# Performance work log

Measured on AMD Instinct MI355X. Metric: run time of the kernel, lower is better.

The kernel has to match this reference:

```python
import jax, jax.numpy as jnp
import numpy as np

D_MODEL = 1024


def setup_inputs() -> dict:
    key = jax.random.key(0)
    k1, k2, k3, k4, k5, k6 = jax.random.split(key, 6)
    B, S, D = 4, 4096, D_MODEL
    scale = 1.0 / np.sqrt(D)
    return {
        "hidden": jax.random.normal(k1, (B, S, D), dtype=jnp.float32),
        "pre_emb": jax.random.normal(k2, (B, S, D), dtype=jnp.float32),
        "w1": jax.random.normal(k3, (D, D), dtype=jnp.float32) * scale,  # [in, out]
        "b1": jax.random.normal(k4, (D,), dtype=jnp.float32) * 0.01,
        "w2": jax.random.normal(k5, (D, D), dtype=jnp.float32) * scale,
        "b2": jax.random.normal(k6, (D,), dtype=jnp.float32) * 0.01,
    }


def reference(hidden, pre_emb, w1, b1, w2, b2):
    # h = Linear1(hidden); i = Linear2(hidden + pre_emb)
    h = jnp.einsum("bsd,de->bse", hidden, w1) + b1            # [B,S,D]
    i = jnp.einsum("bsd,de->bse", hidden + pre_emb, w2) + b2  # [B,S,D]
    attn = jnp.einsum("bqd,bkd->bqk", h, i)                   # [B,S,S]
    return jax.nn.softmax(attn, axis=-1)
```

## Files before the change

### kernel.cpp

```cpp
#include <hip/hip_runtime.h>
#include <hip/hip_bf16.h>
#include <stdint.h>

#define DM   1024
#define BATCH 4
#define SEQ  4096
#define MTOT (BATCH*SEQ)

typedef __attribute__((ext_vector_type(8))) short bf16x8;
typedef __attribute__((ext_vector_type(4))) float f32x4;

#define GLOAD_LDS16(gp, lp) __builtin_amdgcn_global_load_lds( \
    (const __attribute__((address_space(1))) unsigned int*)(gp), \
    (__attribute__((address_space(3))) unsigned int*)(lp), 16, 0, 0)

__device__ __forceinline__ ushort f2bf(float f){
  uint u = __float_as_uint(f);
  u += 0x7FFFu + ((u >> 16) & 1u);
  return (ushort)(u >> 16);
}
__device__ __forceinline__ float bf2f(ushort b){ return __uint_as_float(((uint)b) << 16); }

__device__ __forceinline__ void split4(const float4 v, ushort4& h4, ushort4& l4){
  h4.x = f2bf(v.x); l4.x = f2bf(v.x - bf2f(h4.x));
  h4.y = f2bf(v.y); l4.y = f2bf(v.y - bf2f(h4.y));
  h4.z = f2bf(v.z); l4.z = f2bf(v.z - bf2f(h4.z));
  h4.w = f2bf(v.w); l4.w = f2bf(v.w - bf2f(h4.w));
}

__global__ __launch_bounds__(256)
void prep_w_split(const float* __restrict__ w1, const float* __restrict__ w2,
                  ushort* __restrict__ w1h, ushort* __restrict__ w1l,
                  ushort* __restrict__ w2h, ushort* __restrict__ w2l){
  const float* w = blockIdx.y ? w2 : w1;
  ushort* oh = blockIdx.y ? w2h : w1h;
  ushort* ol = blockIdx.y ? w2l : w1l;
  size_t off = ((size_t)blockIdx.x * 256 + threadIdx.x) * 4;
  float4 v = *(const float4*)&w[off];
  ushort4 h4, l4; split4(v, h4, l4);
  *(ushort4*)&oh[off] = h4;
  *(ushort4*)&ol[off] = l4;
}

__global__ __launch_bounds__(256)
void prep_xy(const float* __restrict__ hidden, const float* __restrict__ pre,
             ushort* __restrict__ xh, ushort* __restrict__ xl,
             ushort* __restrict__ yh, ushort* __restrict__ yl, int writeX){
  size_t off = ((size_t)blockIdx.x * 256 + threadIdx.x) * 4;
  float4 h = *(const float4*)&hidden[off];
  float4 p = *(const float4*)&pre[off];
  float4 y = {h.x + p.x, h.y + p.y, h.z + p.z, h.w + p.w};
  ushort4 a, b;
  if (writeX){
    split4(h, a, b);
    *(ushort4*)&xh[off] = a;
    *(ushort4*)&xl[off] = b;
  }
  split4(y, a, b);
  *(ushort4*)&yh[off] = a;
  *(ushort4*)&yl[off] = b;
}

__global__ __launch_bounds__(256)
void c2k(const float* __restrict__ w2, const float* __restrict__ b1,
         float* __restrict__ c2){
  const int wid = threadIdx.x >> 6, lane = threadIdx.x & 63;
  const int row = blockIdx.x * 4 + wid;
  float s = 0.f;
  #pragma unroll
  for (int t = 0; t < 16; t++){
    int e = lane + 64 * t;
    s += w2[(size_t)row * DM + e] * b1[e];
  }
  #pragma unroll
  for (int o = 32; o > 0; o >>= 1) s += __shfl_xor(s, o, 64);
  if (lane == 0) c2[row] = s;
}

__global__ __launch_bounds__(256)
void betak(const ushort* __restrict__ yh, const ushort* __restrict__ yl,
           const float* __restrict__ c2, float* __restrict__ beta){
  const int wid = threadIdx.x >> 6, lane = threadIdx.x & 63;
  const size_t r = (size_t)blockIdx.x * 4 + wid;
  const size_t base = r * DM + lane * 16;
  float s = 0.f;
  #pragma unroll
  for (int q = 0; q < 2; q++){
    bf16x8 h = *(const bf16x8*)&yh[base + q * 8];
    bf16x8 l = *(const bf16x8*)&yl[base + q * 8];
    float4 c0 = *(const float4*)&c2[lane * 16 + q * 8];
    float4 c1 = *(const float4*)&c2[lane * 16 + q * 8 + 4];
    s += (bf2f((ushort)h[0]) + bf2f((ushort)l[0])) * c0.x;
    s += (bf2f((ushort)h[1]) + bf2f((ushort)l[1])) * c0.y;
    s += (bf2f((ushort)h[2]) + bf2f((ushort)l[2])) * c0.z;
    s += (bf2f((ushort)h[3]) + bf2f((ushort)l[3])) * c0.w;
    s += (bf2f((ushort)h[4]) + bf2f((ushort)l[4])) * c1.x;
    s += (bf2f((ushort)h[5]) + bf2f((ushort)l[5])) * c1.y;
    s += (bf2f((ushort)h[6]) + bf2f((ushort)l[6])) * c1.z;
    s += (bf2f((ushort)h[7]) + bf2f((ushort)l[7])) * c1.w;
  }
  #pragma unroll
  for (int o = 32; o > 0; o >>= 1) s += __shfl_xor(s, o, 64);
  if (lane == 0) beta[r] = s;
}

__device__ __forceinline__ void bt_mainloop(
    const ushort* __restrict__ Aph, const ushort* __restrict__ Apl,
    const ushort* __restrict__ Bph, const ushort* __restrict__ Bpl,
    int m0, int n0, f32x4 (&acc)[4][4]){
  __shared__ alignas(16) ushort Ah[128*32];
  __shared__ alignas(16) ushort Al[128*32];
  __shared__ alignas(16) ushort Bh[128*32];
  __shared__ alignas(16) ushort Bl[128*32];

  const int tid = threadIdx.x;
  const int lane = tid & 63, wid = tid >> 6;
  const int wm = (wid & 1) * 64, wn = (wid >> 1) * 64;
  const int lr = lane & 15, lk = (lane >> 4) * 8;

  const ushort* plane = (wid == 0) ? Aph : (wid == 1) ? Apl : (wid == 2) ? Bph : Bpl;
  ushort* lds = (wid == 0) ? Ah : (wid == 1) ? Al : (wid == 2) ? Bh : Bl;
  const int r0 = (wid < 2) ? m0 : n0;
  const size_t goff = (size_t)(r0 + (lane >> 2)) * DM + (lane & 3) * 8;

  for (int k0 = 0; k0 < DM; k0 += 32){
    __syncthreads();
    const ushort* gp = plane + goff + k0;
    #pragma unroll
    for (int t = 0; t < 8; t++){
      GLOAD_LDS16(gp + (size_t)t * 16 * DM, lds + t * 512);
    }
    __syncthreads();

    bf16x8 fah[4], fal[4], fbh[4], fbl[4];
    #pragma unroll
    for (int i = 0; i < 4; i++){
      fah[i] = *(const bf16x8*)&Ah[(wm + i*16 + lr)*32 + lk];
      fal[i] = *(const bf16x8*)&Al[(wm + i*16 + lr)*32 + lk];
      fbh[i] = *(const bf16x8*)&Bh[(wn + i*16 + lr)*32 + lk];
      fbl[i] = *(const bf16x8*)&Bl[(wn + i*16 + lr)*32 + lk];
    }
    #pragma unroll
    for (int i = 0; i < 4; i++)
      #pragma unroll
      for (int j = 0; j < 4; j++){
        acc[i][j] = __builtin_amdgcn_mfma_f32_16x16x32_bf16(fah[i], fbh[j], acc[i][j], 0, 0, 0);
        acc[i][j] = __builtin_amdgcn_mfma_f32_16x16x32_bf16(fah[i], fbl[j], acc[i][j], 0, 0, 0);
        acc[i][j] = __builtin_amdgcn_mfma_f32_16x16x32_bf16(fal[i], fbh[j], acc[i][j], 0, 0, 0);
      }
  }
}

__global__ __launch_bounds__(256, 2)
void gemm_bt_split(const ushort* __restrict__ Aph, const ushort* __restrict__ Apl,
                   const ushort* __restrict__ Bph, const ushort* __restrict__ Bpl,
                   ushort* __restrict__ oh, ushort* __restrict__ ol){
  const int m0 = blockIdx.y * 128, n0 = blockIdx.x * 128;
  f32x4 acc[4][4];
  for (int i = 0; i < 4; i++) for (int j = 0; j < 4; j++) acc[i][j] = (f32x4){0.f,0.f,0.f,0.f};
  bt_mainloop(Aph, Apl, Bph, Bpl, m0, n0, acc);

  const int lane = threadIdx.x & 63, wid = threadIdx.x >> 6;
  const int wm = (wid & 1) * 64, wn = (wid >> 1) * 64;
  const int lr = lane & 15;
  const int rbase = (lane >> 4) * 4;
  #pragma unroll
  for (int i = 0; i < 4; i++)
    #pragma unroll
    for (int j = 0; j < 4; j++){
      int gc = n0 + wn + j*16 + lr;
      #pragma unroll
      for (int r = 0; r < 4; r++){
        int gr = m0 + wm + i*16 + rbase + r;
        float v = acc[i][j][r];
        ushort hb = f2bf(v);
        size_t o = (size_t)gr * DM + gc;
        oh[o] = hb;
        ol[o] = f2bf(v - bf2f(hb));
      }
    }
}

__global__ __launch_bounds__(256, 2)
void gemm_bt_f32(const ushort* __restrict__ Aph, const ushort* __restrict__ Apl,
                 const ushort* __restrict__ Bph, const ushort* __restrict__ Bpl,
                 float* __restrict__ out){
  const int b = blockIdx.y;
  const int id = blockIdx.x;
  const int c = id & 7;
  const int m = (id >> 3) & 63;
  const int s = m >> 3, u = m & 7;
  const int g = id >> 9;
  const int qt = 16*g + 8*(c & 1) + s;
  const int kt = 8*(c >> 1) + u;
  const int m0 = qt * 128, n0 = kt * 128;
  const size_t abase = (size_t)b * SEQ * DM;

  f32x4 acc[4][4];
  for (int i = 0; i < 4; i++) for (int j = 0; j < 4; j++) acc[i][j] = (f32x4){0.f,0.f,0.f,0.f};
  bt_mainloop(Aph + abase, Apl + abase, Bph + abase, Bpl + abase, m0, n0, acc);

  const int lane = threadIdx.x & 63, wid = threadIdx.x >> 6;
  const int wm = (wid & 1) * 64, wn = (wid >> 1) * 64;
  const int lr = lane & 15;
  const int rbase = (lane >> 4) * 4;
  #pragma unroll
  for (int i = 0; i < 4; i++)
    #pragma unroll
    for (int j = 0; j < 4; j++){
      int gc = n0 + wn + j*16 + lr;
      #pragma unroll
      for (int r = 0; r < 4; r++){
        int gr = m0 + wm + i*16 + rbase + r;
        __builtin_nontemporal_store(acc[i][j][r],
            &out[((size_t)b * SEQ + gr) * SEQ + gc]);
      }
    }
}

#define ASTR 40
__global__ __launch_bounds__(256, 2)
void gemm_z_manual(const float* __restrict__ hidden,
                   const ushort* __restrict__ gth, const ushort* __restrict__ gtl,
                   ushort* __restrict__ zh, ushort* __restrict__ zl){
  const int m0 = blockIdx.y * 128, n0 = blockIdx.x * 128;
  __shared__ alignas(16) ushort Ah[128*ASTR];
  __shared__ alignas(16) ushort Al[128*ASTR];
  __shared__ alignas(16) ushort Bh[128*32];
  __shared__ alignas(16) ushort Bl[128*32];

  const int tid = threadIdx.x;
  const int lane = tid & 63, wid = tid >> 6;
  const int wm = (wid & 1) * 64, wn = (wid >> 1) * 64;
  const int lr = lane & 15, lk = (lane >> 4) * 8;

  const ushort* bp = (wid < 2) ? gth : gtl;
  ushort* blds = (wid < 2) ? Bh : Bl;
  const int tb = (wid & 1) * 4;
  const size_t bgoff = (size_t)(n0 + (lane >> 2)) * DM + (lane & 3) * 8;

  f32x4 acc[4][4];
  for (int i = 0; i < 4; i++) for (int j = 0; j < 4; j++) acc[i][j] = (f32x4){0.f,0.f,0.f,0.f};

  for (int k0 = 0; k0 < DM; k0 += 32){
    __syncthreads();
    const ushort* gb = bp + bgoff + k0;
    #pragma unroll
    for (int t = 0; t < 4; t++){
      GLOAD_LDS16(gb + (size_t)(tb + t) * 16 * DM, blds + (tb + t) * 512);
    }
    #pragma unroll
    for (int c = 0; c < 4; c++){
      int idx = c * 256 + tid;
      int row = idx >> 3, kq = (idx & 7) * 4;
      size_t ga = (size_t)(m0 + row) * DM + k0 + kq;
      float4 v = *(const float4*)&hidden[ga];
      ushort4 h4, l4;
      split4(v, h4, l4);
      *(ushort4*)&Ah[row*ASTR + kq] = h4;
      *(ushort4*)&Al[row*ASTR + kq] = l4;
    }
    __syncthreads();

    bf16x8 fah[4], fal[4], fbh[4], fbl[4];
    #pragma unroll
    for (int i = 0; i < 4; i++){
      fah[i] = *(const bf16x8*)&Ah[(wm + i*16 + lr)*ASTR + lk];
      fal[i] = *(const bf16x8*)&Al[(wm + i*16 + lr)*ASTR + lk];
      fbh[i] = *(const bf16x8*)&Bh[(wn + i*16 + lr)*32 + lk];
      fbl[i] = *(const bf16x8*)&Bl[(wn + i*16 + lr)*32 + lk];
    }
    #pragma unroll
    for (int i = 0; i < 4; i++)
      #pragma unroll
      for (int j = 0; j < 4; j++){
        acc[i][j] = __builtin_amdgcn_mfma_f32_16x16x32_bf16(fah[i], fbh[j], acc[i][j], 0, 0, 0);
        acc[i][j] = __builtin_amdgcn_mfma_f32_16x16x32_bf16(fah[i], fbl[j], acc[i][j], 0, 0, 0);
        acc[i][j] = __builtin_amdgcn_mfma_f32_16x16x32_bf16(fal[i], fbh[j], acc[i][j], 0, 0, 0);
      }
  }

  const int rbase = (lane >> 4) * 4;
  #pragma unroll
  for (int i = 0; i < 4; i++)
    #pragma unroll
    for (int j = 0; j < 4; j++){
      int gc = n0 + wn + j*16 + lr;
      #pragma unroll
      for (int r = 0; r < 4; r++){
        int gr = m0 + wm + i*16 + rbase + r;
        float v = acc[i][j][r];
        ushort hb = f2bf(v);
        size_t o = (size_t)gr * DM + gc;
        zh[o] = hb;
        zl[o] = f2bf(v - bf2f(hb));
      }
    }
}

__global__ __launch_bounds__(256)
void softmax_rows(float* __restrict__ out, const float* __restrict__ beta){
  __shared__ float red[8];
  const size_t row = blockIdx.x;
  float* p = out + row * (size_t)SEQ;
  const float* bp = beta + ((row >> 12) << 12);
  const int tid = threadIdx.x, lane = tid & 63, wid = tid >> 6;

  f32x4 v[4];
  float m = -3.0e38f;
  #pragma unroll
  for (int c = 0; c < 4; c++){
    v[c] = __builtin_nontemporal_load(((const f32x4*)p) + c*256 + tid);
    f32x4 bb = *(((const f32x4*)bp) + c*256 + tid);
    v[c] += bb;
    m = fmaxf(m, fmaxf(fmaxf(v[c].x, v[c].y), fmaxf(v[c].z, v[c].w)));
  }
  #pragma unroll
  for (int o = 32; o > 0; o >>= 1) m = fmaxf(m, __shfl_xor(m, o, 64));
  if (lane == 0) red[wid] = m;
  __syncthreads();
  const float M = fmaxf(fmaxf(red[0], red[1]), fmaxf(red[2], red[3]));

  float s = 0.f;
  #pragma unroll
  for (int c = 0; c < 4; c++){
    v[c].x = __expf(v[c].x - M); s += v[c].x;
    v[c].y = __expf(v[c].y - M); s += v[c].y;
    v[c].z = __expf(v[c].z - M); s += v[c].z;
    v[c].w = __expf(v[c].w - M); s += v[c].w;
  }
  #pragma unroll
  for (int o = 32; o > 0; o >>= 1) s += __shfl_xor(s, o, 64);
  if (lane == 0) red[4 + wid] = s;
  __syncthreads();
  const float inv = 1.0f / (red[4] + red[5] + red[6] + red[7]);
  #pragma unroll
  for (int c = 0; c < 4; c++){
    v[c] *= inv;
    __builtin_nontemporal_store(v[c], ((f32x4*)p) + c*256 + tid);
  }
}

extern "C" void kernel_launch(void* const* d_in, const int* in_sizes, int n_in,
                              void* d_out, int out_size, void* d_ws, size_t ws_size,
                              hipStream_t stream){
  const float* hidden = (const float*)d_in[0];
  const float* pre    = (const float*)d_in[1];
  const float* w1     = (const float*)d_in[2];
  const float* b1     = (const float*)d_in[3];
  const float* w2     = (const float*)d_in[4];
  float* out = (float*)d_out;

  char* ws = (char*)d_ws;
  const size_t WP = (size_t)DM * DM * sizeof(ushort);
  const size_t AP = (size_t)MTOT * DM * sizeof(ushort);
  const bool big = ws_size >= 6*AP + 6*WP + (1u << 20);

  ushort *w1h, *w1l, *w2h, *w2l, *Gth, *Gtl, *Xh, *Xl, *Yh, *Yl, *Zh, *Zl;
  float *c2, *beta;
  if (big){
    Xh  = (ushort*)(ws + 0*AP);  Xl  = (ushort*)(ws + 1*AP);
    Yh  = (ushort*)(ws + 2*AP);  Yl  = (ushort*)(ws + 3*AP);
    Zh  = (ushort*)(ws + 4*AP);  Zl  = (ushort*)(ws + 5*AP);
    w1h = (ushort*)(ws + 6*AP);          w1l = (ushort*)(ws + 6*AP + WP);
    w2h = (ushort*)(ws + 6*AP + 2*WP);   w2l = (ushort*)(ws + 6*AP + 3*WP);
    Gth = (ushort*)(ws + 6*AP + 4*WP);   Gtl = (ushort*)(ws + 6*AP + 5*WP);
    c2   = (float*)(ws + 6*AP + 6*WP);
    beta = c2 + DM;
  } else {
    Zh  = (ushort*)(ws + 0*AP);  Zl  = (ushort*)(ws + 1*AP);
    Yh  = (ushort*)(ws + 2*AP);  Yl  = (ushort*)(ws + 3*AP);
    Gth = (ushort*)(ws + 4*AP);  Gtl = (ushort*)(ws + 4*AP + WP);
    w1h = (ushort*)(ws + 0);       w1l = (ushort*)(ws + WP);
    w2h = (ushort*)(ws + 2*WP);    w2l = (ushort*)(ws + 3*WP);
    c2   = (float*)(ws + 4*AP + 2*WP);
    beta = c2 + DM;
    Xh = Xl = nullptr;
  }

  prep_w_split<<<dim3(1024, 2), 256, 0, stream>>>(w1, w2, w1h, w1l, w2h, w2l);
  prep_xy<<<dim3(16384), 256, 0, stream>>>(hidden, pre, Xh, Xl, Yh, Yl, big ? 1 : 0);
  c2k<<<dim3(256), 256, 0, stream>>>(w2, b1, c2);
  gemm_bt_split<<<dim3(8, 8), 256, 0, stream>>>(w2h, w2l, w1h, w1l, Gth, Gtl);
  if (big){
    gemm_bt_split<<<dim3(8, 128), 256, 0, stream>>>(Xh, Xl, Gth, Gtl, Zh, Zl);
  } else {
    gemm_z_manual<<<dim3(8, 128), 256, 0, stream>>>(hidden, Gth, Gtl, Zh, Zl);
  }
  betak<<<dim3(4096), 256, 0, stream>>>(Yh, Yl, c2, beta);
  gemm_bt_f32<<<dim3(1024, BATCH), 256, 0, stream>>>(Zh, Zl, Yh, Yl, out);
  softmax_rows<<<dim3(MTOT), 256, 0, stream>>>(out, beta);
}
```

Before: 958.0 us.

## Fuse beta reduction into prep_xy and XOR-swizzle LDS tiles in GEMMs

The beta row-dot with c2 is now computed inside prep_xy from the fp32 sum, so the separate betak kernel and its second pass over the Y planes go away. c2k is moved before prep_xy to satisfy the dependency. Separately, the bt_mainloop and gemm_z B-tile global-to-LDS loads and fragment reads use an XOR swizzle on the k-chunk index to reduce LDS bank conflicts. The swizzle must match on both the write and read side, and beta is now computed from the unsplit fp32 values.

```diff
diff --git a/kernel.cpp b/kernel.cpp
--- a/kernel.cpp
+++ b/kernel.cpp
@@ -45,8 +45,11 @@
 __global__ __launch_bounds__(256)
 void prep_xy(const float* __restrict__ hidden, const float* __restrict__ pre,
              ushort* __restrict__ xh, ushort* __restrict__ xl,
-             ushort* __restrict__ yh, ushort* __restrict__ yl, int writeX){
-  size_t off = ((size_t)blockIdx.x * 256 + threadIdx.x) * 4;
+             ushort* __restrict__ yh, ushort* __restrict__ yl,
+             const float* __restrict__ c2, float* __restrict__ beta, int writeX){
+  __shared__ float red[4];
+  const int tid = threadIdx.x, lane = tid & 63, wid = tid >> 6;
+  size_t off = ((size_t)blockIdx.x * 256 + tid) * 4;
   float4 h = *(const float4*)&hidden[off];
   float4 p = *(const float4*)&pre[off];
   float4 y = {h.x + p.x, h.y + p.y, h.z + p.z, h.w + p.w};
@@ -59,6 +62,14 @@
   split4(y, a, b);
   *(ushort4*)&yh[off] = a;
   *(ushort4*)&yl[off] = b;
+
+  float4 c = *(const float4*)&c2[tid * 4];
+  float s = y.x * c.x + y.y * c.y + y.z * c.z + y.w * c.w;
+  #pragma unroll
+  for (int o = 32; o > 0; o >>= 1) s += __shfl_xor(s, o, 64);
+  if (lane == 0) red[wid] = s;
+  __syncthreads();
+  if (tid == 0) beta[blockIdx.x] = red[0] + red[1] + red[2] + red[3];
 }
 
 __global__ __launch_bounds__(256)
@@ -75,33 +86,6 @@
   #pragma unroll
   for (int o = 32; o > 0; o >>= 1) s += __shfl_xor(s, o, 64);
   if (lane == 0) c2[row] = s;
-}
-
-__global__ __launch_bounds__(256)
-void betak(const ushort* __restrict__ yh, const ushort* __restrict__ yl,
-           const float* __restrict__ c2, float* __restrict__ beta){
-  const int wid = threadIdx.x >> 6, lane = threadIdx.x & 63;
-  const size_t r = (size_t)blockIdx.x * 4 + wid;
-  const size_t base = r * DM + lane * 16;
-  float s = 0.f;
-  #pragma unroll
-  for (int q = 0; q < 2; q++){
-    bf16x8 h = *(const bf16x8*)&yh[base + q * 8];
-    bf16x8 l = *(const bf16x8*)&yl[base + q * 8];
-    float4 c0 = *(const float4*)&c2[lane * 16 + q * 8];
-    float4 c1 = *(const float4*)&c2[lane * 16 + q * 8 + 4];
-    s += (bf2f((ushort)h[0]) + bf2f((ushort)l[0])) * c0.x;
-    s += (bf2f((ushort)h[1]) + bf2f((ushort)l[1])) * c0.y;
-    s += (bf2f((ushort)h[2]) + bf2f((ushort)l[2])) * c0.z;
-    s += (bf2f((ushort)h[3]) + bf2f((ushort)l[3])) * c0.w;
-    s += (bf2f((ushort)h[4]) + bf2f((ushort)l[4])) * c1.x;
-    s += (bf2f((ushort)h[5]) + bf2f((ushort)l[5])) * c1.y;
-    s += (bf2f((ushort)h[6]) + bf2f((ushort)l[6])) * c1.z;
-    s += (bf2f((ushort)h[7]) + bf2f((ushort)l[7])) * c1.w;
-  }
-  #pragma unroll
-  for (int o = 32; o > 0; o >>= 1) s += __shfl_xor(s, o, 64);
-  if (lane == 0) beta[r] = s;
 }
 
 __device__ __forceinline__ void bt_mainloop(
@@ -116,12 +100,14 @@
   const int tid = threadIdx.x;
   const int lane = tid & 63, wid = tid >> 6;
   const int wm = (wid & 1) * 64, wn = (wid >> 1) * 64;
-  const int lr = lane & 15, lk = (lane >> 4) * 8;
+  const int lr = lane & 15;
+  const int lks = (((lane >> 4) ^ ((lane >> 1) & 3)) << 3);
 
   const ushort* plane = (wid == 0) ? Aph : (wid == 1) ? Apl : (wid == 2) ? Bph : Bpl;
   ushort* lds = (wid == 0) ? Ah : (wid == 1) ? Al : (wid == 2) ? Bh : Bl;
   const int r0 = (wid < 2) ? m0 : n0;
-  const size_t goff = (size_t)(r0 + (lane >> 2)) * DM + (lane & 3) * 8;
+  const size_t goff = (size_t)(r0 + (lane >> 2)) * DM
+                    + (size_t)(((lane & 3) ^ ((lane >> 3) & 3)) * 8);
 
   for (int k0 = 0; k0 < DM; k0 += 32){
     __syncthreads();
@@ -135,10 +121,10 @@
     bf16x8 fah[4], fal[4], fbh[4], fbl[4];
     #pragma unroll
     for (int i = 0; i < 4; i++){
-      fah[i] = *(const bf16x8*)&Ah[(wm + i*16 + lr)*32 + lk];
-      fal[i] = *(const bf16x8*)&Al[(wm + i*16 + lr)*32 + lk];
-      fbh[i] = *(const bf16x8*)&Bh[(wn + i*16 + lr)*32 + lk];
-      fbl[i] = *(const bf16x8*)&Bl[(wn + i*16 + lr)*32 + lk];
+      fah[i] = *(const bf16x8*)&Ah[(wm + i*16 + lr)*32 + lks];
+      fal[i] = *(const bf16x8*)&Al[(wm + i*16 + lr)*32 + lks];
+      fbh[i] = *(const bf16x8*)&Bh[(wn + i*16 + lr)*32 + lks];
+      fbl[i] = *(const bf16x8*)&Bl[(wn + i*16 + lr)*32 + lks];
     }
     #pragma unroll
     for (int i = 0; i < 4; i++)
@@ -233,11 +219,13 @@
   const int lane = tid & 63, wid = tid >> 6;
   const int wm = (wid & 1) * 64, wn = (wid >> 1) * 64;
   const int lr = lane & 15, lk = (lane >> 4) * 8;
+  const int lks = (((lane >> 4) ^ ((lane >> 1) & 3)) << 3);
 
   const ushort* bp = (wid < 2) ? gth : gtl;
   ushort* blds = (wid < 2) ? Bh : Bl;
   const int tb = (wid & 1) * 4;
-  const size_t bgoff = (size_t)(n0 + (lane >> 2)) * DM + (lane & 3) * 8;
+  const size_t bgoff = (size_t)(n0 + (lane >> 2)) * DM
+                     + (size_t)(((lane & 3) ^ ((lane >> 3) & 3)) * 8);
 
   f32x4 acc[4][4];
   for (int i = 0; i < 4; i++) for (int j = 0; j < 4; j++) acc[i][j] = (f32x4){0.f,0.f,0.f,0.f};
@@ -267,8 +255,8 @@
     for (int i = 0; i < 4; i++){
       fah[i] = *(const bf16x8*)&Ah[(wm + i*16 + lr)*ASTR + lk];
       fal[i] = *(const bf16x8*)&Al[(wm + i*16 + lr)*ASTR + lk];
-      fbh[i] = *(const bf16x8*)&Bh[(wn + i*16 + lr)*32 + lk];
-      fbl[i] = *(const bf16x8*)&Bl[(wn + i*16 + lr)*32 + lk];
+      fbh[i] = *(const bf16x8*)&Bh[(wn + i*16 + lr)*32 + lks];
+      fbl[i] = *(const bf16x8*)&Bl[(wn + i*16 + lr)*32 + lks];
     }
     #pragma unroll
     for (int i = 0; i < 4; i++)
@@ -379,15 +367,14 @@
   }
 
   prep_w_split<<<dim3(1024, 2), 256, 0, stream>>>(w1, w2, w1h, w1l, w2h, w2l);
-  prep_xy<<<dim3(16384), 256, 0, stream>>>(hidden, pre, Xh, Xl, Yh, Yl, big ? 1 : 0);
   c2k<<<dim3(256), 256, 0, stream>>>(w2, b1, c2);
+  prep_xy<<<dim3(16384), 256, 0, stream>>>(hidden, pre, Xh, Xl, Yh, Yl, c2, beta, big ? 1 : 0);
   gemm_bt_split<<<dim3(8, 8), 256, 0, stream>>>(w2h, w2l, w1h, w1l, Gth, Gtl);
   if (big){
     gemm_bt_split<<<dim3(8, 128), 256, 0, stream>>>(Xh, Xl, Gth, Gtl, Zh, Zl);
   } else {
     gemm_z_manual<<<dim3(8, 128), 256, 0, stream>>>(hidden, Gth, Gtl, Zh, Zl);
   }
-  betak<<<dim3(4096), 256, 0, stream>>>(Yh, Yl, c2, beta);
   gemm_bt_f32<<<dim3(1024, BATCH), 256, 0, stream>>>(Zh, Zl, Yh, Yl, out);
   softmax_rows<<<dim3(MTOT), 256, 0, stream>>>(out, beta);
 }
```

Result: faster. 936.3 us (-2.3%).
